# Optimization experiments

Measured on AMD Instinct MI355X. Metric: run time of the kernel, lower is better.

## Reference

```python
import jax, jax.numpy as jnp
import numpy as np

B, S, IN, HID, OUT = 8, 4096, 128, 128, 1

def setup_inputs() -> dict:
    key = jax.random.key(0)
    ks = jax.random.split(key, 16)
    xav = lambda k, i, o: jax.random.normal(k, (i, o), jnp.float32) * np.sqrt(2.0 / (i + o))
    return {
        'x': jax.random.normal(ks[0], (B, S, IN), jnp.float32),
        'm1': xav(ks[1], IN, HID), 'b1': jnp.zeros((1, 1, HID), jnp.float32),
        'm2': xav(ks[2], HID, HID), 'b2': jnp.zeros((1, 1, HID), jnp.float32),
        'wq': xav(ks[3], HID, HID), 'wk': xav(ks[4], HID, HID), 'wv': xav(ks[5], HID, HID),
        'ml0': xav(ks[6], 128, 64), 'bl0': jnp.zeros((1, 1, 64), jnp.float32),
        'ml1': xav(ks[7], 64, 32), 'bl1': jnp.zeros((1, 1, 32), jnp.float32),
        'm3': xav(ks[8], 32, OUT), 'b3': jnp.zeros((1, 1, OUT), jnp.float32),
        'atten_size': 5,
    }

def reference(x, m1, b1, m2, b2, wq, wk, wv, ml0, bl0, ml1, bl1, m3, b3, atten_size):
    a = atten_size
    h = jax.nn.relu(x @ m1 + b1)
    h = jax.nn.relu(h @ m2 + b2)            # [B,S,H]
    vals = h @ wv
    pad_cfg = ((0, 0), (a, a), (0, 0))
    padded = jnp.pad(h, pad_cfg)
    padded_v = jnp.pad(vals, pad_cfg)
    # window gather via roll, matching torch.roll(padded, k, 1) for k=-a..a, then slice
    x_nei = jnp.stack([jnp.roll(padded, k, axis=1) for k in range(-a, a + 1)], axis=2)[:, a:-a]   # [B,S,W,H]
    v_nei = jnp.stack([jnp.roll(padded_v, k, axis=1) for k in range(-a, a + 1)], axis=2)[:, a:-a]
    keys = x_nei @ wk                        # [B,S,W,H]
    query = h @ wq                           # [B,S,H]
    scale = 1.0 / np.sqrt(float(HID))
    dot = jnp.einsum('bswh,bsh->bsw', keys, query) * scale
    atten_w = jax.nn.softmax(dot, axis=2)    # [B,S,W]
    o = jnp.einsum('bsw,bswh->bsh', atten_w, v_nei)
    o = jax.nn.relu(o @ ml0 + bl0)
    o = jax.nn.relu(o @ ml1 + bl1)
    o = jax.nn.sigmoid(o @ m3 + b3)          # [B,S,OUT]
    return (o, atten_w)
```

## Files before the change

kernel.cpp:

```cpp
#include <hip/hip_runtime.h>
#include <hip/hip_bf16.h>
#include <math.h>

#define SEQ 4096
#define NB 8
#define CHUNK 64
#define HALO 5
#define WIN 11
#define MROWS 80
#define AROWS 74
#define HSTR 136
#define VSTR 72
#define NT 512
#define CNT 256

typedef short s16x8 __attribute__((ext_vector_type(8)));
typedef float f32x4 __attribute__((ext_vector_type(4)));

#define WAVE_SYNC() asm volatile("s_waitcnt lgkmcnt(0)" ::: "memory")

__device__ __forceinline__ unsigned short f2bf(float f) {
    return __builtin_bit_cast(unsigned short, __float2bfloat16(f));
}

#define OFF_M1  0
#define OFF_M2  16384
#define OFF_WQK 32768
#define OFF_WF  49152
#define OFF_ML1 57344
#define WS_ELEMS 59392

__global__ void convert_weights(const float* __restrict__ m1, const float* __restrict__ m2,
                                const float* __restrict__ wq, const float* __restrict__ wk,
                                const float* __restrict__ wv, const float* __restrict__ ml0,
                                const float* __restrict__ ml1, unsigned short* __restrict__ ws)
{
    int idx = blockIdx.x * CNT + threadIdx.x;
    if (idx < 16384) {
        ws[idx] = f2bf(m1[(idx & 127) * 128 + (idx >> 7)]);
    } else if (idx < 32768) {
        int r = idx - 16384;
        ws[idx] = f2bf(m2[(r & 127) * 128 + (r >> 7)]);
    } else if (idx < 49152) {
        int r = idx - 32768;
        int d = r >> 7, e = r & 127;
        const float4* qa = (const float4*)(wq + e * 128);
        const float4* ka = (const float4*)(wk + d * 128);
        float a0 = 0.f, a1 = 0.f, a2 = 0.f, a3 = 0.f;
        #pragma unroll
        for (int c = 0; c < 32; ++c) {
            float4 A = qa[c], B = ka[c];
            a0 = fmaf(A.x, B.x, a0); a1 = fmaf(A.y, B.y, a1);
            a2 = fmaf(A.z, B.z, a2); a3 = fmaf(A.w, B.w, a3);
        }
        ws[idx] = f2bf((a0 + a1 + a2 + a3) * 0.08838834764831845f);
    } else if (idx < 57344) {
        int r = idx - 49152;
        int n = r >> 7, k = r & 127;
        const float* vr = wv + k * 128;
        float a = 0.f;
        #pragma unroll
        for (int c = 0; c < 128; ++c) a = fmaf(vr[c], ml0[c * 64 + n], a);
        ws[idx] = f2bf(a);
    } else if (idx < WS_ELEMS) {
        int r = idx - 57344;
        int n = r >> 6, k = r & 63;
        ws[idx] = f2bf(ml1[k * 32 + n]);
    }
}

__device__ __forceinline__ void loadB4(s16x8 d[4], const unsigned short* __restrict__ wt,
                                       int ct, int l15, int hi)
{
    const unsigned short* p = wt + (ct * 16 + l15) * 128 + hi * 8;
    d[0] = *(const s16x8*)(p);
    d[1] = *(const s16x8*)(p + 32);
    d[2] = *(const s16x8*)(p + 64);
    d[3] = *(const s16x8*)(p + 96);
}

template<int MT, bool RELU, bool BIAS>
__device__ __forceinline__ void gemmS(const unsigned short* __restrict__ src,
                                      const s16x8 bf[4],
                                      const float* __restrict__ bias,
                                      unsigned short* __restrict__ dst,
                                      int l15, int hi, int wave)
{
    f32x4 acc[MT];
    #pragma unroll
    for (int i = 0; i < MT; ++i) acc[i] = (f32x4){0.f, 0.f, 0.f, 0.f};
    const unsigned short* arow = src + l15 * HSTR + hi * 8;
    #pragma unroll
    for (int ks = 0; ks < 4; ++ks)
        #pragma unroll
        for (int rt = 0; rt < MT; ++rt) {
            s16x8 a = *(const s16x8*)(arow + rt * 16 * HSTR + ks * 32);
            acc[rt] = __builtin_amdgcn_mfma_f32_16x16x32_bf16(a, bf[ks], acc[rt], 0, 0, 0);
        }
    const int c = wave * 16 + l15;
    const float bb = BIAS ? bias[c] : 0.f;
    #pragma unroll
    for (int rt = 0; rt < MT; ++rt)
        #pragma unroll
        for (int j = 0; j < 4; ++j) {
            float v = acc[rt][j] + bb;
            if (RELU) v = fmaxf(v, 0.f);
            dst[(rt * 16 + hi * 4 + j) * HSTR + c] = f2bf(v);
        }
}

__global__ __launch_bounds__(NT, 4)
void ExLRestSelfAtten_mfma(const float* __restrict__ x,
                           const float* __restrict__ b1, const float* __restrict__ b2,
                           const float* __restrict__ bl0, const float* __restrict__ bl1,
                           const float* __restrict__ m3, const float* __restrict__ b3,
                           const unsigned short* __restrict__ wsw,
                           float* __restrict__ out0, float* __restrict__ attw)
{
    __shared__ __align__(16) unsigned short bufA[MROWS * HSTR];
    __shared__ __align__(16) unsigned short bufB[MROWS * HSTR];
    __shared__ __align__(16) unsigned short qbuf[CHUNK * HSTR];
    __shared__ __align__(16) float sband[4 * 16 * 12];
    __shared__ __align__(16) float saw [CHUNK * WIN];

    unsigned short* o2b = bufA;

    const int t = threadIdx.x;
    const int lane = t & 63, wave = t >> 6;
    const int l15 = lane & 15, hi = lane >> 4, rl = hi * 4;
    const int bx = blockIdx.x;
    const int b = bx >> 6;
    const int cstart = (bx & 63) * CHUNK;

    s16x8 wA[4], wB[4];
    loadB4(wA, wsw + OFF_M1, wave, l15, hi);

    const float* xb = x + (size_t)b * SEQ * 128;
    for (int idx = t; idx < MROWS * 32; idx += NT) {
        int r = idx >> 5, k4 = (idx & 31) << 2;
        int p = cstart - HALO + r;
        float4 v = make_float4(0.f, 0.f, 0.f, 0.f);
        if (r < AROWS && p >= 0 && p < SEQ) v = *(const float4*)(xb + (size_t)p * 128 + k4);
        ushort4 o;
        o.x = f2bf(v.x); o.y = f2bf(v.y); o.z = f2bf(v.z); o.w = f2bf(v.w);
        *(ushort4*)(bufA + r * HSTR + k4) = o;
    }
    __syncthreads();

    loadB4(wB, wsw + OFF_M2, wave, l15, hi);
    gemmS<5, true, true>(bufA, wA, b1, bufB, l15, hi, wave);
    __syncthreads();

    loadB4(wA, wsw + OFF_WQK, wave, l15, hi);
    gemmS<5, true, true>(bufB, wB, b2, bufA, l15, hi, wave);
    __syncthreads();

    loadB4(wB, wsw + OFF_WF, wave & 3, l15, hi);
    gemmS<4, false, false>(bufA + HALO * HSTR, wA, nullptr, qbuf, l15, hi, wave);
    {
        const int cg = wave & 3, rh = wave >> 2;
        const int rt0 = rh ? 3 : 0, ntr = rh ? 2 : 3;
        f32x4 acc[3];
        #pragma unroll
        for (int i = 0; i < 3; ++i) acc[i] = (f32x4){0.f, 0.f, 0.f, 0.f};
        const unsigned short* arow = bufA + (rt0 * 16 + l15) * HSTR + hi * 8;
        #pragma unroll
        for (int ks = 0; ks < 4; ++ks)
            for (int rt = 0; rt < ntr; ++rt) {
                s16x8 a = *(const s16x8*)(arow + rt * 16 * HSTR + ks * 32);
                acc[rt] = __builtin_amdgcn_mfma_f32_16x16x32_bf16(a, wB[ks], acc[rt], 0, 0, 0);
            }
        const int c = cg * 16 + l15;
        for (int rt = 0; rt < ntr; ++rt)
            #pragma unroll
            for (int j = 0; j < 4; ++j)
                bufB[((rt0 + rt) * 16 + hi * 4 + j) * HSTR + c] = f2bf(acc[rt][j]);
    }
    __syncthreads();

    s16x8 wml1[2][2];
    float bl1a, bl1b, m3a, m3b, b3v;
    if (wave < 4) {
        const int rt = wave;
        s16x8 aq[4];
        #pragma unroll
        for (int ks = 0; ks < 4; ++ks)
            aq[ks] = *(const s16x8*)(qbuf + (rt * 16 + l15) * HSTR + ks * 32 + hi * 8);
        f32x4 s0 = (f32x4){0.f, 0.f, 0.f, 0.f}, s1 = s0;
        #pragma unroll
        for (int ks = 0; ks < 4; ++ks) {
            s16x8 k0 = *(const s16x8*)(bufA + (rt * 16 + l15) * HSTR + ks * 32 + hi * 8);
            s16x8 k1 = *(const s16x8*)(bufA + ((rt + 1) * 16 + l15) * HSTR + ks * 32 + hi * 8);
            s0 = __builtin_amdgcn_mfma_f32_16x16x32_bf16(aq[ks], k0, s0, 0, 0, 0);
            s1 = __builtin_amdgcn_mfma_f32_16x16x32_bf16(aq[ks], k1, s1, 0, 0, 0);
        }
        float* sb = sband + rt * 192;
        #pragma unroll
        for (int j = 0; j < 4; ++j) {
            int w0 = rl + j + 10 - l15;
            if (w0 >= 0 && w0 <= 10) sb[(rl + j) * 12 + w0] = s0[j];
        }
        #pragma unroll
        for (int j = 0; j < 4; ++j) {
            int w1 = rl + j - 6 - l15;
            if (w1 >= 0 && w1 <= 10) sb[(rl + j) * 12 + w1] = s1[j];
        }
        WAVE_SYNC();
        if (hi == 0) {
            const float* sr = sb + l15 * 12;
            float d[WIN], mx = -1e30f;
            #pragma unroll
            for (int w = 0; w < WIN; ++w) { d[w] = sr[w]; mx = fmaxf(mx, d[w]); }
            float sum = 0.f;
            #pragma unroll
            for (int w = 0; w < WIN; ++w) { d[w] = __expf(d[w] - mx); sum += d[w]; }
            float inv = 1.f / sum;
            const int s = rt * 16 + l15;
            float* ab = attw + (size_t)(b * SEQ + cstart + s) * WIN;
            #pragma unroll
            for (int w = 0; w < WIN; ++w) {
                float a = d[w] * inv;
                saw[s * WIN + w] = a;
                ab[w] = a;
            }
        }
        const unsigned short* p0 = wsw + OFF_ML1 + l15 * 64 + hi * 8;
        const unsigned short* p1 = wsw + OFF_ML1 + (16 + l15) * 64 + hi * 8;
        wml1[0][0] = *(const s16x8*)(p0); wml1[0][1] = *(const s16x8*)(p0 + 32);
        wml1[1][0] = *(const s16x8*)(p1); wml1[1][1] = *(const s16x8*)(p1 + 32);
        bl1a = bl1[l15]; bl1b = bl1[16 + l15];
        m3a = m3[l15];   m3b = m3[16 + l15];
        b3v = b3[0];
    }
    __syncthreads();

    {
        const int s = t >> 3, c0 = (t & 7) << 3;
        float acc[8] = {0.f,0.f,0.f,0.f,0.f,0.f,0.f,0.f};
        #pragma unroll
        for (int w = 0; w < WIN; ++w) {
            float aw = saw[s * WIN + w];
            uint4 u = *(const uint4*)(bufB + (s + 10 - w) * HSTR + c0);
            unsigned uu[4] = {u.x, u.y, u.z, u.w};
            #pragma unroll
            for (int q = 0; q < 4; ++q) {
                acc[2 * q]     = fmaf(aw, __builtin_bit_cast(float, uu[q] << 16), acc[2 * q]);
                acc[2 * q + 1] = fmaf(aw, __builtin_bit_cast(float, uu[q] & 0xffff0000u), acc[2 * q + 1]);
            }
        }
        float4 bv0 = *(const float4*)(bl0 + c0);
        float4 bv1 = *(const float4*)(bl0 + c0 + 4);
        const float bb[8] = {bv0.x, bv0.y, bv0.z, bv0.w, bv1.x, bv1.y, bv1.z, bv1.w};
        unsigned short pk[8];
        #pragma unroll
        for (int i = 0; i < 8; ++i) pk[i] = f2bf(fmaxf(acc[i] + bb[i], 0.f));
        uint4 ov;
        ov.x = pk[0] | ((unsigned)pk[1] << 16); ov.y = pk[2] | ((unsigned)pk[3] << 16);
        ov.z = pk[4] | ((unsigned)pk[5] << 16); ov.w = pk[6] | ((unsigned)pk[7] << 16);
        *(uint4*)(o2b + s * VSTR + c0) = ov;
    }
    __syncthreads();

    if (wave < 4) {
        const int ot = wave;
        s16x8 ao[2];
        #pragma unroll
        for (int ks = 0; ks < 2; ++ks)
            ao[ks] = *(const s16x8*)(o2b + (ot * 16 + l15) * VSTR + ks * 32 + hi * 8);
        f32x4 h0 = (f32x4){0.f, 0.f, 0.f, 0.f}, h1 = h0;
        #pragma unroll
        for (int ks = 0; ks < 2; ++ks) {
            h0 = __builtin_amdgcn_mfma_f32_16x16x32_bf16(ao[ks], wml1[0][ks], h0, 0, 0, 0);
            h1 = __builtin_amdgcn_mfma_f32_16x16x32_bf16(ao[ks], wml1[1][ks], h1, 0, 0, 0);
        }
        float* ob = out0 + (size_t)b * SEQ + cstart + ot * 16;
        #pragma unroll
        for (int j = 0; j < 4; ++j) {
            float v0 = fmaxf(h0[j] + bl1a, 0.f);
            float v1 = fmaxf(h1[j] + bl1b, 0.f);
            float con = v0 * m3a + v1 * m3b;
            con += __shfl_xor(con, 1, 64);
            con += __shfl_xor(con, 2, 64);
            con += __shfl_xor(con, 4, 64);
            con += __shfl_xor(con, 8, 64);
            if (l15 == 0)
                ob[rl + j] = 1.f / (1.f + __expf(-(con + b3v)));
        }
    }
}

extern "C" void kernel_launch(void* const* d_in, const int* in_sizes, int n_in,
                              void* d_out, int out_size, void* d_ws, size_t ws_size,
                              hipStream_t stream)
{
    const float* x   = (const float*)d_in[0];
    const float* m1  = (const float*)d_in[1];
    const float* b1  = (const float*)d_in[2];
    const float* m2  = (const float*)d_in[3];
    const float* b2  = (const float*)d_in[4];
    const float* wq  = (const float*)d_in[5];
    const float* wk  = (const float*)d_in[6];
    const float* wv  = (const float*)d_in[7];
    const float* ml0 = (const float*)d_in[8];
    const float* bl0 = (const float*)d_in[9];
    const float* ml1 = (const float*)d_in[10];
    const float* bl1 = (const float*)d_in[11];
    const float* m3  = (const float*)d_in[12];
    const float* b3  = (const float*)d_in[13];

    float* out0 = (float*)d_out;
    float* attw = out0 + (size_t)NB * SEQ;

    unsigned short* wsw = (unsigned short*)d_ws;
    convert_weights<<<(WS_ELEMS + CNT - 1) / CNT, CNT, 0, stream>>>(
        m1, m2, wq, wk, wv, ml0, ml1, wsw);
    ExLRestSelfAtten_mfma<<<NB * (SEQ / CHUNK), NT, 0, stream>>>(
        x, b1, b2, bl0, bl1, m3, b3, wsw, out0, attw);
}
```

Measured before the change: 26.99 us.

## Double chunk to 128 rows and make attention tail wave-local

Each block now processes 128 sequence positions instead of 64, so the 10-row halo recompute of the two MLP layers is a smaller share of the work, and the grid shrinks to 256 blocks. All 8 waves now own 16 rows each through scores, softmax, weighted sum and the output MLP. This replaces block-wide barriers with per-wave LDS waits and reuses qbuf for the intermediate. The trade-off is larger LDS use and lower occupancy (launch bounds 2). With only 256 blocks, some CUs may sit underfilled.

```diff
diff --git a/kernel.cpp b/kernel.cpp
--- a/kernel.cpp
+++ b/kernel.cpp
@@ -4,13 +4,12 @@
 
 #define SEQ 4096
 #define NB 8
-#define CHUNK 64
+#define CHUNK 128
 #define HALO 5
 #define WIN 11
-#define MROWS 80
-#define AROWS 74
+#define MROWS 144
+#define AROWS 138
 #define HSTR 136
-#define VSTR 72
 #define NT 512
 #define CNT 256
 
@@ -109,7 +108,7 @@
         }
 }
 
-__global__ __launch_bounds__(NT, 4)
+__global__ __launch_bounds__(NT, 2)
 void ExLRestSelfAtten_mfma(const float* __restrict__ x,
                            const float* __restrict__ b1, const float* __restrict__ b2,
                            const float* __restrict__ bl0, const float* __restrict__ bl1,
@@ -120,17 +119,14 @@
     __shared__ __align__(16) unsigned short bufA[MROWS * HSTR];
     __shared__ __align__(16) unsigned short bufB[MROWS * HSTR];
     __shared__ __align__(16) unsigned short qbuf[CHUNK * HSTR];
-    __shared__ __align__(16) float sband[4 * 16 * 12];
-    __shared__ __align__(16) float saw [CHUNK * WIN];
-
-    unsigned short* o2b = bufA;
+    __shared__ __align__(16) float sband[8 * 16 * 12];
 
     const int t = threadIdx.x;
     const int lane = t & 63, wave = t >> 6;
     const int l15 = lane & 15, hi = lane >> 4, rl = hi * 4;
     const int bx = blockIdx.x;
-    const int b = bx >> 6;
-    const int cstart = (bx & 63) * CHUNK;
+    const int b = bx >> 5;
+    const int cstart = (bx & 31) * CHUNK;
 
     s16x8 wA[4], wB[4];
     loadB4(wA, wsw + OFF_M1, wave, l15, hi);
@@ -148,21 +144,21 @@
     __syncthreads();
 
     loadB4(wB, wsw + OFF_M2, wave, l15, hi);
-    gemmS<5, true, true>(bufA, wA, b1, bufB, l15, hi, wave);
+    gemmS<9, true, true>(bufA, wA, b1, bufB, l15, hi, wave);
     __syncthreads();
 
     loadB4(wA, wsw + OFF_WQK, wave, l15, hi);
-    gemmS<5, true, true>(bufB, wB, b2, bufA, l15, hi, wave);
+    gemmS<9, true, true>(bufB, wB, b2, bufA, l15, hi, wave);
     __syncthreads();
 
     loadB4(wB, wsw + OFF_WF, wave & 3, l15, hi);
-    gemmS<4, false, false>(bufA + HALO * HSTR, wA, nullptr, qbuf, l15, hi, wave);
+    gemmS<8, false, false>(bufA + HALO * HSTR, wA, nullptr, qbuf, l15, hi, wave);
     {
         const int cg = wave & 3, rh = wave >> 2;
-        const int rt0 = rh ? 3 : 0, ntr = rh ? 2 : 3;
-        f32x4 acc[3];
-        #pragma unroll
-        for (int i = 0; i < 3; ++i) acc[i] = (f32x4){0.f, 0.f, 0.f, 0.f};
+        const int rt0 = rh ? 5 : 0, ntr = rh ? 4 : 5;
+        f32x4 acc[5];
+        #pragma unroll
+        for (int i = 0; i < 5; ++i) acc[i] = (f32x4){0.f, 0.f, 0.f, 0.f};
         const unsigned short* arow = bufA + (rt0 * 16 + l15) * HSTR + hi * 8;
         #pragma unroll
         for (int ks = 0; ks < 4; ++ks)
@@ -176,104 +172,115 @@
             for (int j = 0; j < 4; ++j)
                 bufB[((rt0 + rt) * 16 + hi * 4 + j) * HSTR + c] = f2bf(acc[rt][j]);
     }
-    __syncthreads();
-
     s16x8 wml1[2][2];
-    float bl1a, bl1b, m3a, m3b, b3v;
-    if (wave < 4) {
-        const int rt = wave;
-        s16x8 aq[4];
-        #pragma unroll
-        for (int ks = 0; ks < 4; ++ks)
-            aq[ks] = *(const s16x8*)(qbuf + (rt * 16 + l15) * HSTR + ks * 32 + hi * 8);
-        f32x4 s0 = (f32x4){0.f, 0.f, 0.f, 0.f}, s1 = s0;
-        #pragma unroll
-        for (int ks = 0; ks < 4; ++ks) {
-            s16x8 k0 = *(const s16x8*)(bufA + (rt * 16 + l15) * HSTR + ks * 32 + hi * 8);
-            s16x8 k1 = *(const s16x8*)(bufA + ((rt + 1) * 16 + l15) * HSTR + ks * 32 + hi * 8);
-            s0 = __builtin_amdgcn_mfma_f32_16x16x32_bf16(aq[ks], k0, s0, 0, 0, 0);
-            s1 = __builtin_amdgcn_mfma_f32_16x16x32_bf16(aq[ks], k1, s1, 0, 0, 0);
-        }
-        float* sb = sband + rt * 192;
-        #pragma unroll
-        for (int j = 0; j < 4; ++j) {
-            int w0 = rl + j + 10 - l15;
-            if (w0 >= 0 && w0 <= 10) sb[(rl + j) * 12 + w0] = s0[j];
-        }
-        #pragma unroll
-        for (int j = 0; j < 4; ++j) {
-            int w1 = rl + j - 6 - l15;
-            if (w1 >= 0 && w1 <= 10) sb[(rl + j) * 12 + w1] = s1[j];
-        }
-        WAVE_SYNC();
-        if (hi == 0) {
-            const float* sr = sb + l15 * 12;
-            float d[WIN], mx = -1e30f;
-            #pragma unroll
-            for (int w = 0; w < WIN; ++w) { d[w] = sr[w]; mx = fmaxf(mx, d[w]); }
-            float sum = 0.f;
-            #pragma unroll
-            for (int w = 0; w < WIN; ++w) { d[w] = __expf(d[w] - mx); sum += d[w]; }
-            float inv = 1.f / sum;
-            const int s = rt * 16 + l15;
-            float* ab = attw + (size_t)(b * SEQ + cstart + s) * WIN;
-            #pragma unroll
-            for (int w = 0; w < WIN; ++w) {
-                float a = d[w] * inv;
-                saw[s * WIN + w] = a;
-                ab[w] = a;
-            }
-        }
+    {
         const unsigned short* p0 = wsw + OFF_ML1 + l15 * 64 + hi * 8;
         const unsigned short* p1 = wsw + OFF_ML1 + (16 + l15) * 64 + hi * 8;
         wml1[0][0] = *(const s16x8*)(p0); wml1[0][1] = *(const s16x8*)(p0 + 32);
         wml1[1][0] = *(const s16x8*)(p1); wml1[1][1] = *(const s16x8*)(p1 + 32);
-        bl1a = bl1[l15]; bl1b = bl1[16 + l15];
-        m3a = m3[l15];   m3b = m3[16 + l15];
-        b3v = b3[0];
-    }
+    }
+    const float bl1a = bl1[l15], bl1b = bl1[16 + l15];
+    const float m3a = m3[l15],   m3b = m3[16 + l15];
+    const float b3v = b3[0];
     __syncthreads();
 
-    {
-        const int s = t >> 3, c0 = (t & 7) << 3;
-        float acc[8] = {0.f,0.f,0.f,0.f,0.f,0.f,0.f,0.f};
+    float* sb = sband + wave * 192;
+    {
+        s16x8 aq[4];
+        #pragma unroll
+        for (int ks = 0; ks < 4; ++ks)
+            aq[ks] = *(const s16x8*)(qbuf + (wave * 16 + l15) * HSTR + ks * 32 + hi * 8);
+        f32x4 s0 = (f32x4){0.f, 0.f, 0.f, 0.f}, s1 = s0;
+        #pragma unroll
+        for (int ks = 0; ks < 4; ++ks) {
+            s16x8 k0 = *(const s16x8*)(bufA + (wave * 16 + l15) * HSTR + ks * 32 + hi * 8);
+            s16x8 k1 = *(const s16x8*)(bufA + ((wave + 1) * 16 + l15) * HSTR + ks * 32 + hi * 8);
+            s0 = __builtin_amdgcn_mfma_f32_16x16x32_bf16(aq[ks], k0, s0, 0, 0, 0);
+            s1 = __builtin_amdgcn_mfma_f32_16x16x32_bf16(aq[ks], k1, s1, 0, 0, 0);
+        }
+        #pragma unroll
+        for (int j = 0; j < 4; ++j) {
+            int w0 = rl + j + 10 - l15;
+            if (w0 >= 0 && w0 <= 10) sb[(rl + j) * 12 + w0] = s0[j];
+        }
+        #pragma unroll
+        for (int j = 0; j < 4; ++j) {
+            int w1 = rl + j - 6 - l15;
+            if (w1 >= 0 && w1 <= 10) sb[(rl + j) * 12 + w1] = s1[j];
+        }
+    }
+    WAVE_SYNC();
+
+    if (hi == 0) {
+        float* sr = sb + l15 * 12;
+        float d[WIN], mx = -1e30f;
+        #pragma unroll
+        for (int w = 0; w < WIN; ++w) { d[w] = sr[w]; mx = fmaxf(mx, d[w]); }
+        float sum = 0.f;
+        #pragma unroll
+        for (int w = 0; w < WIN; ++w) { d[w] = __expf(d[w] - mx); sum += d[w]; }
+        float inv = 1.f / sum;
+        float* ab = attw + (size_t)(b * SEQ + cstart + wave * 16 + l15) * WIN;
         #pragma unroll
         for (int w = 0; w < WIN; ++w) {
-            float aw = saw[s * WIN + w];
-            uint4 u = *(const uint4*)(bufB + (s + 10 - w) * HSTR + c0);
-            unsigned uu[4] = {u.x, u.y, u.z, u.w};
+            float a = d[w] * inv;
+            sr[w] = a;
+            ab[w] = a;
+        }
+    }
+    WAVE_SYNC();
+
+    {
+        const int sl = lane >> 2, c0 = (lane & 3) << 4;
+        const int s = wave * 16 + sl;
+        float oc[16];
+        #pragma unroll
+        for (int i = 0; i < 16; ++i) oc[i] = 0.f;
+        #pragma unroll
+        for (int w = 0; w < WIN; ++w) {
+            float aw = sb[sl * 12 + w];
+            const unsigned short* vr = bufB + (s + 10 - w) * HSTR + c0;
+            uint4 u0 = *(const uint4*)(vr);
+            uint4 u1 = *(const uint4*)(vr + 8);
+            unsigned uu[8] = {u0.x, u0.y, u0.z, u0.w, u1.x, u1.y, u1.z, u1.w};
             #pragma unroll
-            for (int q = 0; q < 4; ++q) {
-                acc[2 * q]     = fmaf(aw, __builtin_bit_cast(float, uu[q] << 16), acc[2 * q]);
-                acc[2 * q + 1] = fmaf(aw, __builtin_bit_cast(float, uu[q] & 0xffff0000u), acc[2 * q + 1]);
+            for (int q = 0; q < 8; ++q) {
+                oc[2 * q]     = fmaf(aw, __builtin_bit_cast(float, uu[q] << 16), oc[2 * q]);
+                oc[2 * q + 1] = fmaf(aw, __builtin_bit_cast(float, uu[q] & 0xffff0000u), oc[2 * q + 1]);
             }
         }
         float4 bv0 = *(const float4*)(bl0 + c0);
         float4 bv1 = *(const float4*)(bl0 + c0 + 4);
-        const float bb[8] = {bv0.x, bv0.y, bv0.z, bv0.w, bv1.x, bv1.y, bv1.z, bv1.w};
-        unsigned short pk[8];
-        #pragma unroll
-        for (int i = 0; i < 8; ++i) pk[i] = f2bf(fmaxf(acc[i] + bb[i], 0.f));
-        uint4 ov;
-        ov.x = pk[0] | ((unsigned)pk[1] << 16); ov.y = pk[2] | ((unsigned)pk[3] << 16);
-        ov.z = pk[4] | ((unsigned)pk[5] << 16); ov.w = pk[6] | ((unsigned)pk[7] << 16);
-        *(uint4*)(o2b + s * VSTR + c0) = ov;
-    }
-    __syncthreads();
-
-    if (wave < 4) {
-        const int ot = wave;
+        float4 bv2 = *(const float4*)(bl0 + c0 + 8);
+        float4 bv3 = *(const float4*)(bl0 + c0 + 12);
+        const float bb[16] = {bv0.x, bv0.y, bv0.z, bv0.w, bv1.x, bv1.y, bv1.z, bv1.w,
+                              bv2.x, bv2.y, bv2.z, bv2.w, bv3.x, bv3.y, bv3.z, bv3.w};
+        unsigned short pk[16];
+        #pragma unroll
+        for (int i = 0; i < 16; ++i) pk[i] = f2bf(fmaxf(oc[i] + bb[i], 0.f));
+        uint4 ov0, ov1;
+        ov0.x = pk[0] | ((unsigned)pk[1] << 16);  ov0.y = pk[2] | ((unsigned)pk[3] << 16);
+        ov0.z = pk[4] | ((unsigned)pk[5] << 16);  ov0.w = pk[6] | ((unsigned)pk[7] << 16);
+        ov1.x = pk[8] | ((unsigned)pk[9] << 16);  ov1.y = pk[10] | ((unsigned)pk[11] << 16);
+        ov1.z = pk[12] | ((unsigned)pk[13] << 16); ov1.w = pk[14] | ((unsigned)pk[15] << 16);
+        unsigned short* od = qbuf + s * HSTR + c0;
+        *(uint4*)(od) = ov0;
+        *(uint4*)(od + 8) = ov1;
+    }
+    WAVE_SYNC();
+
+    {
         s16x8 ao[2];
         #pragma unroll
         for (int ks = 0; ks < 2; ++ks)
-            ao[ks] = *(const s16x8*)(o2b + (ot * 16 + l15) * VSTR + ks * 32 + hi * 8);
+            ao[ks] = *(const s16x8*)(qbuf + (wave * 16 + l15) * HSTR + ks * 32 + hi * 8);
         f32x4 h0 = (f32x4){0.f, 0.f, 0.f, 0.f}, h1 = h0;
         #pragma unroll
         for (int ks = 0; ks < 2; ++ks) {
             h0 = __builtin_amdgcn_mfma_f32_16x16x32_bf16(ao[ks], wml1[0][ks], h0, 0, 0, 0);
             h1 = __builtin_amdgcn_mfma_f32_16x16x32_bf16(ao[ks], wml1[1][ks], h1, 0, 0, 0);
         }
-        float* ob = out0 + (size_t)b * SEQ + cstart + ot * 16;
+        float* ob = out0 + (size_t)b * SEQ + cstart + wave * 16;
         #pragma unroll
         for (int j = 0; j < 4; ++j) {
             float v0 = fmaxf(h0[j] + bl1a, 0.f);
```

Measured after the change: 28.34 us. 1.05x slower.
